# Performance work log

Measured on AMD Instinct MI355X. Metric: run time of the kernel, lower is better.

The kernel has to match this reference:

```python
import jax, jax.numpy as jnp
import numpy as np

N_NODES = 50000
N_EDGES = 800000
N_GRAPHS = 512
F_IN = 64
HID = 64
OUT = 1
NUM_LAYERS = 3


def setup_inputs() -> dict:
    key = jax.random.key(0)
    ks = jax.random.split(key, 10)
    x = jax.random.normal(ks[0], (N_NODES, F_IN), dtype=jnp.float32)
    edge_index = jax.random.randint(ks[1], (2, N_EDGES), 0, N_NODES, dtype=jnp.int64)
    batch = jnp.sort(jax.random.randint(ks[2], (N_NODES,), 0, N_GRAPHS, dtype=jnp.int64))
    def glorot(k, shape):
        lim = np.sqrt(6.0 / (shape[0] + shape[1]))
        return jax.random.uniform(k, shape, jnp.float32, -lim, lim)
    W1 = glorot(ks[3], (F_IN, HID))
    b1 = jnp.zeros((HID,), jnp.float32)
    W2 = glorot(ks[4], (HID, HID))
    b2 = jnp.zeros((HID,), jnp.float32)
    Wmem = glorot(ks[5], (HID, OUT))
    bmem = jnp.zeros((OUT,), jnp.float32)
    Wtime = glorot(ks[6], (HID, OUT))
    btime = jnp.zeros((OUT,), jnp.float32)
    return {"x": x, "edge_index": edge_index, "batch": batch,
            "W1": W1, "b1": b1, "W2": W2, "b2": b2,
            "Wmem": Wmem, "bmem": bmem, "Wtime": Wtime, "btime": btime}


def _gcn_forward(x, edge_index, batch, W1, b1, W2, b2, Wmem, bmem, Wtime, btime):
    N = x.shape[0]
    # add self-loops (PyG GCNConv default)
    loop = jnp.arange(N, dtype=edge_index.dtype)
    src = jnp.concatenate([edge_index[0], loop])  # [E+N]
    dst = jnp.concatenate([edge_index[1], loop])
    # symmetric normalization: deg over destination nodes (incl. self-loops)
    deg = jax.ops.segment_sum(jnp.ones_like(dst, dtype=x.dtype), dst, num_segments=N)
    dinv = jnp.where(deg > 0, jax.lax.rsqrt(deg), 0.0)
    norm = (dinv[src] * dinv[dst])[:, None]  # [E+N, 1]

    def conv(h, W, b):
        h = h @ W                                   # transform first (PyG order)
        msg = h[src] * norm                         # gather + normalize
        agg = jax.ops.segment_sum(msg, dst, num_segments=N)  # scatter-add
        return agg + b

    h = jax.nn.relu(conv(x, W1, b1))
    for _ in range(NUM_LAYERS - 1):
        h = jax.nn.relu(conv(h, W2, b2))

    # global_mean_pool over batch index
    sums = jax.ops.segment_sum(h, batch, num_segments=N_GRAPHS)
    cnts = jax.ops.segment_sum(jnp.ones((N,), h.dtype), batch, num_segments=N_GRAPHS)
    pooled = sums / jnp.maximum(cnts, 1.0)[:, None]  # [G, HID]

    mem_pred = (pooled @ Wmem + bmem).squeeze()
    time_pred = (pooled @ Wtime + btime).squeeze()
    return mem_pred, time_pred


def reference(x, edge_index, batch, W1, b1, W2, b2, Wmem, bmem, Wtime, btime):
    return _gcn_forward(x, edge_index, batch, W1, b1, W2, b2, Wmem, bmem, Wtime, btime)
```

## Files before the change

kernel.cpp:

```cpp
#include <hip/hip_runtime.h>
#include <hip/hip_bf16.h>
#include <hip/hip_fp16.h>

#define F 64
#define BSH 7
#define MAXB 512
#define CAPB 4096

typedef short short8 __attribute__((ext_vector_type(8)));
typedef float f32x4  __attribute__((ext_vector_type(4)));
typedef unsigned short ushort_t;

__device__ __forceinline__ unsigned short f2bf(float x) {
    unsigned u = __float_as_uint(x);
    unsigned r = (u + 0x7fff + ((u >> 16) & 1)) >> 16;
    return (unsigned short)r;
}
__device__ __forceinline__ float bf2f(unsigned short h) {
    return __uint_as_float(((unsigned)h) << 16);
}

__global__ void k_prep(const float* __restrict__ W1, const float* __restrict__ W2,
                       short* __restrict__ Wh1, short* __restrict__ Wl1,
                       short* __restrict__ Wh2, short* __restrict__ Wl2,
                       int* __restrict__ bfill,
                       __half* __restrict__ xn, __half* __restrict__ hA,
                       __half* __restrict__ hB, int n,
                       float* __restrict__ pooled, int* __restrict__ cnt, int ng) {
    int b = blockIdx.x, t = threadIdx.x;
    if (b < 4) {
        const float* W = (b < 2) ? W1 : W2;
        short* WhF = (b < 2) ? Wh1 : Wh2;
        short* WlF = (b < 2) ? Wl1 : Wl2;
        int i = (b & 1) * 256 + t;
        int lane = i & 63;
        int ct = i >> 6;
        int tt = ct & 1, c = ct >> 1;
        int j  = c * 16 + (lane & 15);
        int k0 = tt * 32 + (lane >> 4) * 8;
        #pragma unroll
        for (int e = 0; e < 8; ++e) {
            float xv = W[(k0 + e) * F + j];
            unsigned short hi = f2bf(xv);
            WhF[i * 8 + e] = (short)hi;
            WlF[i * 8 + e] = (short)f2bf(xv - bf2f(hi));
        }
    } else if (b == 4) {
        bfill[t]       = t * CAPB;
        bfill[t + 256] = (t + 256) * CAPB;
    } else if (b == 5) {
        if (t < 32)      ((unsigned*)(xn + (size_t)n * F))[t]      = 0u;
        else if (t < 64) ((unsigned*)(hA + (size_t)n * F))[t - 32] = 0u;
        else if (t < 96) ((unsigned*)(hB + (size_t)n * F))[t - 64] = 0u;
    } else {
        int idx = (b - 6) * 256 + t;
        if (idx < ng * F) pooled[idx] = 0.f;
        else if (idx < ng * F + ng) cnt[idx - ng * F] = 0;
    }
}

__global__ void k_binscatter(const int* __restrict__ src, const int* __restrict__ dst,
                             int e, int nbkt, int* __restrict__ bucket_fill,
                             int* __restrict__ binned) {
    __shared__ int h[MAXB], base[MAXB];
    int t = threadIdx.x;
    int perblk = (e + gridDim.x - 1) / gridDim.x;
    int e0 = blockIdx.x * perblk;
    int e1 = min(e0 + perblk, e);
    for (int i = t; i < nbkt; i += 256) h[i] = 0;
    __syncthreads();
    for (int i = e0 + t; i < e1; i += 256) atomicAdd(&h[dst[i] >> BSH], 1);
    __syncthreads();
    for (int i = t; i < nbkt; i += 256) {
        int c = h[i];
        base[i] = c ? atomicAdd(&bucket_fill[i], c) : 0;
        h[i] = 0;
    }
    __syncthreads();
    for (int i = e0 + t; i < e1; i += 256) {
        int d = dst[i];
        int b = d >> BSH;
        int r = atomicAdd(&h[b], 1);
        binned[base[b] + r] = (src[i] << BSH) | (d & ((1 << BSH) - 1));
    }
}

__global__ void k_bincsr(const int* __restrict__ binned, const int* __restrict__ bfill,
                         const float* __restrict__ x, int n,
                         ushort_t* __restrict__ csr, int2* __restrict__ rowse,
                         float* __restrict__ dinv, __half* __restrict__ xn) {
    __shared__ int deg[1 << BSH], dp[1 << BSH], rp[1 << BSH], fill[1 << BSH];
    __shared__ int csr_l[CAPB];
    __shared__ int ovf;
    int b = blockIdx.x;
    int t = threadIdx.x;
    int n0 = b << BSH;
    int nn = min(n - n0, 1 << BSH);
    if (nn <= 0) return;
    int base = b * CAPB;
    int cnt = bfill[b] - base;
    if (t < (1 << BSH)) { deg[t] = 0; fill[t] = 0; }
    for (int i = t; i < CAPB; i += 256) csr_l[i] = n;
    __syncthreads();
    for (int i = t; i < cnt; i += 256) atomicAdd(&deg[binned[base + i] & ((1 << BSH) - 1)], 1);
    __syncthreads();
    if (t < 128) { dp[t] = (deg[t] + 15) & ~15; rp[t] = dp[t]; }
    __syncthreads();
    for (int off = 1; off < 128; off <<= 1) {
        int u = 0;
        if (t < 128 && t >= off) u = rp[t - off];
        __syncthreads();
        if (t < 128) rp[t] += u;
        __syncthreads();
    }
    if (t == 0) ovf = (rp[127] > CAPB);
    __syncthreads();
    if (ovf) {
        if (t < 128) { dp[t] = deg[t]; rp[t] = deg[t]; }
        __syncthreads();
        for (int off = 1; off < 128; off <<= 1) {
            int u = 0;
            if (t < 128 && t >= off) u = rp[t - off];
            __syncthreads();
            if (t < 128) rp[t] += u;
            __syncthreads();
        }
    }
    int total = rp[127];
    for (int i = t; i < cnt; i += 256) {
        int pr = binned[base + i];
        int d = pr & ((1 << BSH) - 1);
        int pos = rp[d] - dp[d] + atomicAdd(&fill[d], 1);
        csr_l[pos] = pr >> BSH;
    }
    __syncthreads();
    for (int i = t; i < total; i += 256) csr[base + i] = (ushort_t)csr_l[i];
    if (t < nn) {
        int start = base + rp[t] - dp[t];
        rowse[n0 + t] = make_int2(start, start + dp[t]);
        dinv[n0 + t]  = rsqrtf((float)(deg[t] + 1));
    }
    for (int i = t; i < nn * 32; i += 256) {
        int r = i >> 5, l = i & 31;
        float dv = rsqrtf((float)(deg[r] + 1));
        float2 v = ((const float2*)(x + (size_t)(n0 + r) * F))[l];
        ((__half2*)(xn + (size_t)(n0 + r) * F))[l] = __floats2half2_rn(v.x * dv, v.y * dv);
    }
}

union SMem {
    struct { short Ah[16][72]; short Al[16][72]; };
    struct { float vals[16][68]; int bids[16]; };
};

template<int MODE>
__global__ __launch_bounds__(256, 8)
void k_layer(const __half* __restrict__ Hn, const int2* __restrict__ rowse,
             const ushort_t* __restrict__ csr, const float* __restrict__ dinv,
             const short* __restrict__ WhF, const short* __restrict__ WlF,
             const float* __restrict__ bias, __half* __restrict__ out,
             const int* __restrict__ batch, float* __restrict__ pooled,
             int* __restrict__ cnt, int n) {
    __shared__ SMem sm;
    __shared__ float sdinv[16];
    int t  = threadIdx.x;
    int w  = t >> 6, t6 = t & 63;
    int g  = t6 >> 5, l = t6 & 31;
    int nb0 = blockIdx.x * 16;
    const __half2* rows = (const __half2*)Hn;

    for (int q = 0; q < 4; ++q) {
        int ndl = w * 4 + q;
        int nd  = nb0 + ndl;
        float ax[8], ay[8];
        #pragma unroll
        for (int i = 0; i < 8; ++i) { ax[i] = 0.f; ay[i] = 0.f; }
        float dn = 0.f;
        if (nd < n) {
            dn = dinv[nd];
            if (g == 0) {
                float2 f = __half22float2(rows[((size_t)nd << 5) + l]);
                ax[0] = f.x; ay[0] = f.y;
            }
            int2 se = rowse[nd];
            int e = se.x, e1 = se.y;
            if ((e & 15) == 0) {
                for (; e + 16 <= e1; e += 16) {
                    int4 cw = *(const int4*)(csr + e + 8 * g);
                    int s[8] = { cw.x & 0xffff, (int)((unsigned)cw.x >> 16),
                                 cw.y & 0xffff, (int)((unsigned)cw.y >> 16),
                                 cw.z & 0xffff, (int)((unsigned)cw.z >> 16),
                                 cw.w & 0xffff, (int)((unsigned)cw.w >> 16) };
                    #pragma unroll
                    for (int i = 0; i < 8; ++i) {
                        float2 f = __half22float2(rows[((size_t)s[i] << 5) + l]);
                        ax[i] += f.x; ay[i] += f.y;
                    }
                }
            }
            if (g == 0) {
                for (; e < e1; ++e) {
                    int s = csr[e];
                    float2 f = __half22float2(rows[((size_t)s << 5) + l]);
                    ax[7] += f.x; ay[7] += f.y;
                }
            }
        }
        float sx = ((ax[0] + ax[1]) + (ax[2] + ax[3])) + ((ax[4] + ax[5]) + (ax[6] + ax[7]));
        float sy = ((ay[0] + ay[1]) + (ay[2] + ay[3])) + ((ay[4] + ay[5]) + (ay[6] + ay[7]));
        sx += __shfl_xor(sx, 32);
        sy += __shfl_xor(sy, 32);
        sx *= dn; sy *= dn;
        if (g == 0) {
            unsigned short hx = f2bf(sx), hy = f2bf(sy);
            *(unsigned*)&sm.Ah[ndl][2 * l] = (unsigned)hx | ((unsigned)hy << 16);
            unsigned short lx = f2bf(sx - bf2f(hx)), ly = f2bf(sy - bf2f(hy));
            *(unsigned*)&sm.Al[ndl][2 * l] = (unsigned)lx | ((unsigned)ly << 16);
            if (l == 0) sdinv[ndl] = dn;
        }
    }
    __syncthreads();

    int c  = w;
    int jj = t6 & 15;
    int kg = t6 >> 4;
    const short8* WhP = (const short8*)WhF;
    const short8* WlP = (const short8*)WlF;
    short8 bh0 = WhP[(c * 2 + 0) * 64 + t6];
    short8 bh1 = WhP[(c * 2 + 1) * 64 + t6];
    short8 bl0 = WlP[(c * 2 + 0) * 64 + t6];
    short8 bl1 = WlP[(c * 2 + 1) * 64 + t6];
    short8 ah0 = *(const short8*)&sm.Ah[jj][kg * 8];
    short8 ah1 = *(const short8*)&sm.Ah[jj][32 + kg * 8];
    short8 al0 = *(const short8*)&sm.Al[jj][kg * 8];
    short8 al1 = *(const short8*)&sm.Al[jj][32 + kg * 8];

    float bv = bias[c * 16 + jj];
    f32x4 acc = {bv, bv, bv, bv};
    acc = __builtin_amdgcn_mfma_f32_16x16x32_bf16(ah0, bh0, acc, 0, 0, 0);
    acc = __builtin_amdgcn_mfma_f32_16x16x32_bf16(ah1, bh1, acc, 0, 0, 0);
    acc = __builtin_amdgcn_mfma_f32_16x16x32_bf16(al0, bh0, acc, 0, 0, 0);
    acc = __builtin_amdgcn_mfma_f32_16x16x32_bf16(al1, bh1, acc, 0, 0, 0);
    acc = __builtin_amdgcn_mfma_f32_16x16x32_bf16(ah0, bl0, acc, 0, 0, 0);
    acc = __builtin_amdgcn_mfma_f32_16x16x32_bf16(ah1, bl1, acc, 0, 0, 0);

    if (MODE == 1) {
        #pragma unroll
        for (int v = 0; v < 4; ++v) {
            int rr = kg * 4 + v;
            int nd = nb0 + rr;
            if (nd < n) {
                float val = fmaxf(acc[v], 0.f) * sdinv[rr];
                out[(size_t)nd * F + c * 16 + jj] = __float2half(val);
            }
        }
    } else {
        __syncthreads();
        #pragma unroll
        for (int v = 0; v < 4; ++v) {
            int rr = kg * 4 + v;
            sm.vals[rr][c * 16 + jj] = fmaxf(acc[v], 0.f);
        }
        if (t < 16) sm.bids[t] = (nb0 + t < n) ? batch[nb0 + t] : -1;
        __syncthreads();
        if (t < 64) {
            float accp = 0.f;
            int curg = sm.bids[0];
            for (int r = 0; r < 16; ++r) {
                int g2 = sm.bids[r];
                if (g2 < 0) break;
                if (g2 != curg) {
                    atomicAdd(&pooled[curg * F + t], accp);
                    curg = g2; accp = 0.f;
                }
                accp += sm.vals[r][t];
            }
            if (curg >= 0) atomicAdd(&pooled[curg * F + t], accp);
        } else if (t == 64) {
            int curg = sm.bids[0], cl = 0;
            for (int r = 0; r < 16; ++r) {
                int g2 = sm.bids[r];
                if (g2 < 0) break;
                if (g2 != curg) { atomicAdd(&cnt[curg], cl); curg = g2; cl = 0; }
                ++cl;
            }
            if (curg >= 0 && cl) atomicAdd(&cnt[curg], cl);
        }
    }
}


__global__ void k_head(const float* __restrict__ pooled, const int* __restrict__ cnt,
                       const float* __restrict__ Wm, const float* __restrict__ bm,
                       const float* __restrict__ Wt, const float* __restrict__ bt,
                       float* __restrict__ out, int g) {
    int gid = (blockIdx.x * blockDim.x + threadIdx.x) >> 6;
    int j = threadIdx.x & 63;
    if (gid >= g) return;
    float c = fmaxf((float)cnt[gid], 1.f);
    float p = pooled[gid * F + j] / c;
    float m = p * Wm[j];
    float t = p * Wt[j];
    #pragma unroll
    for (int off = 32; off > 0; off >>= 1) {
        m += __shfl_down(m, off);
        t += __shfl_down(t, off);
    }
    if (j == 0) {
        out[gid]     = m + bm[0];
        out[g + gid] = t + bt[0];
    }
}


static inline size_t alignup(size_t x) { return (x + 255) & ~(size_t)255; }

extern "C" void kernel_launch(void* const* d_in, const int* in_sizes, int n_in,
                              void* d_out, int out_size, void* d_ws, size_t ws_size,
                              hipStream_t stream) {
    const float* x     = (const float*)d_in[0];
    const int*   eidx  = (const int*)d_in[1];
    const int*   batch = (const int*)d_in[2];
    const float* W1    = (const float*)d_in[3];
    const float* b1    = (const float*)d_in[4];
    const float* W2    = (const float*)d_in[5];
    const float* b2    = (const float*)d_in[6];
    const float* Wm    = (const float*)d_in[7];
    const float* bm    = (const float*)d_in[8];
    const float* Wt    = (const float*)d_in[9];
    const float* bt    = (const float*)d_in[10];
    float* out = (float*)d_out;

    const int N = in_sizes[0] / F;
    const int E = in_sizes[1] / 2;
    const int G = out_size / 2;
    const int* src = eidx;
    const int* dst = eidx + E;
    const int nbkt = (N + (1 << BSH) - 1) >> BSH;

    char* p = (char*)d_ws;
    float*    dinv   = (float*)p;    p += alignup(sizeof(float) * N);
    int2*     rowse  = (int2*)p;     p += alignup(sizeof(int2) * N);
    int*      bfill  = (int*)p;      p += alignup(sizeof(int) * MAXB);
    short*    Wh1    = (short*)p;    p += alignup(sizeof(short) * 4096);
    short*    Wl1    = (short*)p;    p += alignup(sizeof(short) * 4096);
    short*    Wh2    = (short*)p;    p += alignup(sizeof(short) * 4096);
    short*    Wl2    = (short*)p;    p += alignup(sizeof(short) * 4096);
    ushort_t* csr    = (ushort_t*)p; p += alignup(sizeof(ushort_t) * (size_t)nbkt * CAPB);
    int*      binned = (int*)p;      p += alignup(sizeof(int) * (size_t)nbkt * CAPB);
    __half*   xn     = (__half*)p;   p += alignup(sizeof(__half) * (size_t)(N + 1) * F);
    __half*   hA     = (__half*)p;   p += alignup(sizeof(__half) * (size_t)(N + 1) * F);
    __half*   hB     = (__half*)p;   p += alignup(sizeof(__half) * (size_t)(N + 1) * F);
    float*    pooled = (float*)p;    p += alignup(sizeof(float) * G * F);
    int*      cnt    = (int*)p;      p += alignup(sizeof(int) * G);

    const int TB = 256;

    int gPrep = 6 + (G * F + G + TB - 1) / TB;
    k_prep<<<gPrep, TB, 0, stream>>>(W1, W2, Wh1, Wl1, Wh2, Wl2, bfill,
                                     xn, hA, hB, N, pooled, cnt, G);

    k_binscatter<<<128, TB, 0, stream>>>(src, dst, E, nbkt, bfill, binned);
    k_bincsr    <<<nbkt, TB, 0, stream>>>(binned, bfill, x, N, csr, rowse, dinv, xn);

    int gT = (N + 15) / 16;
    k_layer<1><<<gT, TB, 0, stream>>>(xn, rowse, csr, dinv, Wh1, Wl1, b1, hA,
                                      batch, pooled, cnt, N);
    k_layer<1><<<gT, TB, 0, stream>>>(hA, rowse, csr, dinv, Wh2, Wl2, b2, hB,
                                      batch, pooled, cnt, N);
    k_layer<0><<<gT, TB, 0, stream>>>(hB, rowse, csr, dinv, Wh2, Wl2, b2, hA,
                                      batch, pooled, cnt, N);

    int gH = (G * F + TB - 1) / TB;
    k_head<<<gH, TB, 0, stream>>>(pooled, cnt, Wm, bm, Wt, bt, out, G);
}
```

Baseline: 123.1 us.

## Stage bin scatter in shared memory and prefetch CSR indices in aggregation

The binning kernel now uses 512-thread blocks over fixed edge slices. Each block sorts its slice into shared memory by bucket using a block-wide prefix scan, then writes it out contiguously per bucket, so global writes are coalesced instead of scattered. The CSR build now pads only the used part of local memory instead of all CAPB entries, and the layer aggregation loop software-prefetches the next 16-index CSR word. The costs are about 50KB of shared memory per scatter block, which limits occupancy, a binary search per output element, and 64 blocks instead of 128.

```diff
diff --git a/kernel.cpp b/kernel.cpp
--- a/kernel.cpp
+++ b/kernel.cpp
@@ -6,6 +6,7 @@
 #define BSH 7
 #define MAXB 512
 #define CAPB 4096
+#define SLICE 12500
 
 typedef short short8 __attribute__((ext_vector_type(8)));
 typedef float f32x4  __attribute__((ext_vector_type(4)));
@@ -59,29 +60,50 @@
     }
 }
 
-__global__ void k_binscatter(const int* __restrict__ src, const int* __restrict__ dst,
-                             int e, int nbkt, int* __restrict__ bucket_fill,
-                             int* __restrict__ binned) {
-    __shared__ int h[MAXB], base[MAXB];
+__global__ __launch_bounds__(512)
+void k_binscatter(const int* __restrict__ src, const int* __restrict__ dst,
+                  int e, int nbkt, int* __restrict__ bfill,
+                  int* __restrict__ binned) {
+    __shared__ int h[MAXB], pre[MAXB], base[MAXB], cur[MAXB];
+    __shared__ int buf[SLICE];
     int t = threadIdx.x;
-    int perblk = (e + gridDim.x - 1) / gridDim.x;
-    int e0 = blockIdx.x * perblk;
-    int e1 = min(e0 + perblk, e);
-    for (int i = t; i < nbkt; i += 256) h[i] = 0;
-    __syncthreads();
-    for (int i = e0 + t; i < e1; i += 256) atomicAdd(&h[dst[i] >> BSH], 1);
-    __syncthreads();
-    for (int i = t; i < nbkt; i += 256) {
+    int e0 = blockIdx.x * SLICE;
+    int e1 = min(e0 + SLICE, e);
+    int m = e1 - e0;
+    if (m <= 0) return;
+    for (int i = t; i < nbkt; i += 512) h[i] = 0;
+    __syncthreads();
+    for (int i = e0 + t; i < e1; i += 512) atomicAdd(&h[dst[i] >> BSH], 1);
+    __syncthreads();
+    {
+        int v = (t < nbkt) ? h[t] : 0;
+        pre[t] = v;
+        __syncthreads();
+        for (int off = 1; off < 512; off <<= 1) {
+            int u = (t >= off) ? pre[t - off] : 0;
+            __syncthreads();
+            pre[t] += u;
+            __syncthreads();
+        }
+    }
+    for (int i = t; i < nbkt; i += 512) {
         int c = h[i];
-        base[i] = c ? atomicAdd(&bucket_fill[i], c) : 0;
-        h[i] = 0;
-    }
-    __syncthreads();
-    for (int i = e0 + t; i < e1; i += 256) {
+        base[i] = c ? atomicAdd(&bfill[i], c) : 0;
+        cur[i] = pre[i] - c;
+    }
+    __syncthreads();
+    for (int i = e0 + t; i < e1; i += 512) {
         int d = dst[i];
         int b = d >> BSH;
-        int r = atomicAdd(&h[b], 1);
-        binned[base[b] + r] = (src[i] << BSH) | (d & ((1 << BSH) - 1));
+        int slot = atomicAdd(&cur[b], 1);
+        buf[slot] = (src[i] << BSH) | (d & ((1 << BSH) - 1));
+    }
+    __syncthreads();
+    for (int i = t; i < m; i += 512) {
+        int lo = 0, hi = nbkt - 1;
+        while (lo < hi) { int mid = (lo + hi) >> 1; if (pre[mid] <= i) lo = mid + 1; else hi = mid; }
+        int off = i - (pre[lo] - h[lo]);
+        binned[base[lo] + off] = buf[i];
     }
 }
 
@@ -100,7 +122,6 @@
     int base = b * CAPB;
     int cnt = bfill[b] - base;
     if (t < (1 << BSH)) { deg[t] = 0; fill[t] = 0; }
-    for (int i = t; i < CAPB; i += 256) csr_l[i] = n;
     __syncthreads();
     for (int i = t; i < cnt; i += 256) atomicAdd(&deg[binned[base + i] & ((1 << BSH) - 1)], 1);
     __syncthreads();
@@ -127,6 +148,8 @@
         }
     }
     int total = rp[127];
+    for (int i = t; i < total; i += 256) csr_l[i] = n;
+    __syncthreads();
     for (int i = t; i < cnt; i += 256) {
         int pr = binned[base + i];
         int d = pr & ((1 << BSH) - 1);
@@ -184,9 +207,12 @@
             }
             int2 se = rowse[nd];
             int e = se.x, e1 = se.y;
-            if ((e & 15) == 0) {
-                for (; e + 16 <= e1; e += 16) {
-                    int4 cw = *(const int4*)(csr + e + 8 * g);
+            int iters = ((e & 15) == 0) ? ((e1 - e) >> 4) : 0;
+            if (iters > 0) {
+                int4 cw = *(const int4*)(csr + e + 8 * g);
+                for (int it = 0; it < iters; ++it) {
+                    int4 nx = cw;
+                    if (it + 1 < iters) nx = *(const int4*)(csr + e + 16 * (it + 1) + 8 * g);
                     int s[8] = { cw.x & 0xffff, (int)((unsigned)cw.x >> 16),
                                  cw.y & 0xffff, (int)((unsigned)cw.y >> 16),
                                  cw.z & 0xffff, (int)((unsigned)cw.z >> 16),
@@ -196,11 +222,13 @@
                         float2 f = __half22float2(rows[((size_t)s[i] << 5) + l]);
                         ax[i] += f.x; ay[i] += f.y;
                     }
+                    cw = nx;
                 }
             }
+            int er = e + 16 * iters;
             if (g == 0) {
-                for (; e < e1; ++e) {
-                    int s = csr[e];
+                for (; er < e1; ++er) {
+                    int s = csr[er];
                     float2 f = __half22float2(rows[((size_t)s << 5) + l]);
                     ax[7] += f.x; ay[7] += f.y;
                 }
@@ -360,7 +388,8 @@
     k_prep<<<gPrep, TB, 0, stream>>>(W1, W2, Wh1, Wl1, Wh2, Wl2, bfill,
                                      xn, hA, hB, N, pooled, cnt, G);
 
-    k_binscatter<<<128, TB, 0, stream>>>(src, dst, E, nbkt, bfill, binned);
+    int gS = (E + SLICE - 1) / SLICE;
+    k_binscatter<<<gS, 512, 0, stream>>>(src, dst, E, nbkt, bfill, binned);
     k_bincsr    <<<nbkt, TB, 0, stream>>>(binned, bfill, x, N, csr, rowse, dinv, xn);
 
     int gT = (N + 15) / 16;
```

Result: slower. 133.9 us (+8.8%).
